# Performance work log

Hardware: AMD Instinct MI355X
Metric: run time of the kernel (lower is better)

The kernel has to match this reference:

```python
import jax, jax.numpy as jnp
import numpy as np

D = 2048      # d_model
H = 16        # n_heads
DH = 128      # head dim
ROPE = 64     # qk_rope_dim = dh//2
NOPE = 64     # qk_nope_dim = dh//2
QP = 1024     # q_proj_dim = int(D*0.5)
KVP = 1365    # kv_proj_dim = int(D*2/3)
THETA = 10000.0
B, S = 2, 2048


def _ln(x, w, b):
    m = x.mean(-1, keepdims=True)
    v = ((x - m) ** 2).mean(-1, keepdims=True)
    return (x - m) / jnp.sqrt(v + 1e-5) * w + b


def _rot_half(x):
    x1, x2 = jnp.split(x, 2, axis=-1)
    return jnp.concatenate([-x2, x1], axis=-1)


def _rope_tables(seq_len):
    # freqs over full dh (as in torch buffer), then slice first ROPE//2 and repeat(...,2)
    freqs = 1.0 / (THETA ** (jnp.arange(0, DH, 2, dtype=jnp.float32) / DH))  # (DH//2,)
    emb = jnp.arange(seq_len, dtype=jnp.float32)[:, None] * freqs[None, :]   # (S, DH//2)
    c = jnp.cos(emb)[:, : ROPE // 2]
    s = jnp.sin(emb)[:, : ROPE // 2]
    cos = jnp.concatenate([c, c], axis=-1)  # (S, ROPE)  matches .repeat(1,1,1,2)
    sin = jnp.concatenate([s, s], axis=-1)
    return cos, sin


def setup_inputs() -> dict:
    ks = jax.random.split(jax.random.key(0), 8)
    p = lambda i, shape: 0.01 * jax.random.normal(ks[i], shape, dtype=jnp.float32)
    return {
        "query": jax.random.normal(ks[0], (B, S, D), dtype=jnp.float32),
        "W_dq": p(1, (D, QP)),
        "W_uq": p(2, (QP, D)),
        "q_ln_w": jnp.ones((QP,), jnp.float32),
        "q_ln_b": jnp.zeros((QP,), jnp.float32),
        "W_dkv": p(3, (D, KVP + ROPE)),
        "W_ukv": p(4, (KVP, D + H * NOPE)),
        "kv_ln_w": jnp.ones((KVP,), jnp.float32),
        "kv_ln_b": jnp.zeros((KVP,), jnp.float32),
        "W_o": p(5, (D, D)),
    }


def reference(query, W_dq, W_uq, q_ln_w, q_ln_b, W_dkv, W_ukv, kv_ln_w, kv_ln_b, W_o):
    b, sq, _ = query.shape
    # Q low-rank path
    cq = _ln(query @ W_dq, q_ln_w, q_ln_b)                       # (B,S,QP)
    Q = (cq @ W_uq).reshape(b, sq, H, DH).transpose(0, 2, 1, 3)  # (B,H,S,DH)
    Qn, Qr = Q[..., :NOPE], Q[..., NOPE:]
    cos, sin = _rope_tables(sq)                                  # (S,ROPE)
    Qr = Qr * cos + _rot_half(Qr) * sin
    # KV low-rank path
    compressed_kv = query @ W_dkv                                # (B,S,KVP+ROPE)
    kv_lat, Kr = compressed_kv[..., :KVP], compressed_kv[..., KVP:]
    kv_lat = _ln(kv_lat, kv_ln_w, kv_ln_b)
    KV = (kv_lat @ W_ukv).reshape(b, sq, H, DH + NOPE).transpose(0, 2, 1, 3)
    Kn, V = KV[..., :NOPE], KV[..., NOPE:]                       # (B,H,S,NOPE),(B,H,S,DH)
    Kr = Kr * cos + _rot_half(Kr) * sin                          # (B,S,ROPE) shared head
    qh = jnp.concatenate([Qn, Qr], axis=-1)                      # (B,H,S,DH)
    kh = jnp.concatenate([Kn, jnp.broadcast_to(Kr[:, None], (b, H, sq, ROPE))], axis=-1)
    # causal attention, scale 1/sqrt(dh) as in SDPA
    scores = jnp.einsum('bhqd,bhkd->bhqk', qh, kh) / jnp.sqrt(jnp.float32(DH))
    mask = jnp.tril(jnp.ones((sq, sq), dtype=bool))
    scores = jnp.where(mask, scores, -jnp.inf)
    attn = jax.nn.softmax(scores, axis=-1)
    out = jnp.einsum('bhqk,bhkd->bhqd', attn, V).transpose(0, 2, 1, 3).reshape(b, sq, D)
    output = out @ W_o.T                                          # nn.Linear, no bias
    return output, compressed_kv
```

## Files before the change

### kernel.cpp

```cpp
#include <hip/hip_runtime.h>

#define BB_   2
#define S_    2048
#define D_    2048
#define H_    16
#define DH_   128
#define ROPE_ 64
#define QP_   1024
#define KVP_  1365
#define KVPR_ 1429
#define KVP_PAD_ 1408
#define NKV_PAD_ 1536
#define NCOMB_ 2560
#define MT_   4096
#define UKV_N_ 3072

typedef unsigned short u16;
typedef unsigned int   u32;
typedef __attribute__((ext_vector_type(8))) u16    u16x8;
typedef __attribute__((ext_vector_type(8))) __bf16 bf16x8;
typedef __attribute__((ext_vector_type(4))) float  f32x4;

#define NEG_BIG (-1.0e30f)
#define F32_FLAG_BITS 0x49742400u

__device__ __forceinline__ float bf2f(u16 u) {
    u32 x = ((u32)u) << 16;
    return __builtin_bit_cast(float, x);
}
__device__ __forceinline__ u16 f2bf(float f) {
    u32 u = __builtin_bit_cast(u32, f);
    u32 r = u + 0x7fffu + ((u >> 16) & 1u);
    return (u16)(r >> 16);
}
__device__ __forceinline__ bf16x8 ld_bf8(const u16* p) {
    u16x8 v = *(const u16x8*)p;
    return __builtin_bit_cast(bf16x8, v);
}
__device__ __forceinline__ bool flag_f32(const u32* flag) { return flag[0] > F32_FLAG_BITS; }

__device__ __forceinline__ void async16(const void* g, void* l) {
    __builtin_amdgcn_global_load_lds(
        (const __attribute__((address_space(1))) void*)g,
        (__attribute__((address_space(3))) void*)l, 16, 0, 0);
}

__global__ __launch_bounds__(256) void detect_kernel(const u16* __restrict__ q, u32* __restrict__ flag)
{
    u32 m = 0;
    for (int i = blockIdx.x * 256 + threadIdx.x; i < (1 << 20); i += 64 * 256) {
        float v = fabsf(bf2f(q[i]));
        u32 b = __builtin_bit_cast(u32, v);
        m = m > b ? m : b;
    }
    #pragma unroll
    for (int off = 32; off; off >>= 1) {
        u32 o = (u32)__shfl_xor((int)m, off, 64);
        m = m > o ? m : o;
    }
    if ((threadIdx.x & 63) == 0) atomicMax(flag, m);
}

__global__ __launch_bounds__(256) void cast_bf16_kernel(
    const void* __restrict__ in, u16* __restrict__ out, long n, const u32* __restrict__ flag)
{
    bool f32 = flag_f32(flag);
    long i0 = ((long)blockIdx.x * 256 + threadIdx.x) * 8;
    if (i0 >= n) return;
    u16x8 o;
    if (f32) {
        const float* p = (const float*)in + i0;
        #pragma unroll
        for (int j = 0; j < 8; j++) o[j] = f2bf(p[j]);
    } else {
        o = *(const u16x8*)((const u16*)in + i0);
    }
    *(u16x8*)(out + i0) = o;
}

template <int MODE>
__global__ __launch_bounds__(256) void gemm_bt(
    const u16* __restrict__ A, const u16* __restrict__ Bt,
    void* __restrict__ Cout, int M, int N, int K, const u32* __restrict__ flag)
{
    __shared__ u16 As[2][128 * 32];
    __shared__ u16 Bs[2][128 * 32];
    const int tid  = threadIdx.x;
    const int lane = tid & 63;
    const int wave = tid >> 6;
    const int m0 = blockIdx.x * 128;
    const int n0 = blockIdx.y * 128;
    const int wr = (wave >> 1) * 64;
    const int wc = (wave & 1) * 64;
    const bool f32o = (MODE == 2) ? flag_f32(flag) : false;

    const int srow = lane >> 2;
    const int scol = (lane & 3) * 8;
    const u16* aptr0 = A  + (long)(m0 + wave * 32 + srow) * K + scol;
    const u16* bptr0 = Bt + (long)(n0 + wave * 32 + srow) * K + scol;
    const int woff = (wave * 32) * 32;

    f32x4 acc[4][4] = {};

    const int row16 = lane & 15;
    const int kq = (lane >> 4) * 8;

    auto stage = [&](int buf, int kt) {
        u16* asl = &As[buf][woff];
        u16* bsl = &Bs[buf][woff];
        async16(aptr0 + kt,          asl);
        async16(aptr0 + 16 * K + kt, asl + 16 * 32);
        async16(bptr0 + kt,          bsl);
        async16(bptr0 + 16 * K + kt, bsl + 16 * 32);
    };
    auto compute = [&](int buf) {
        bf16x8 a[4], b[4];
        #pragma unroll
        for (int i = 0; i < 4; i++)
            a[i] = ld_bf8(&As[buf][(wr + i * 16 + row16) * 32 + kq]);
        #pragma unroll
        for (int j = 0; j < 4; j++)
            b[j] = ld_bf8(&Bs[buf][(wc + j * 16 + row16) * 32 + kq]);
        #pragma unroll
        for (int i = 0; i < 4; i++)
            #pragma unroll
            for (int j = 0; j < 4; j++)
                acc[i][j] = __builtin_amdgcn_mfma_f32_16x16x32_bf16(a[i], b[j], acc[i][j], 0, 0, 0);
    };

    stage(0, 0);
    __syncthreads();
    const int nk = K >> 5;
    for (int t = 0; t < nk; t += 2) {
        stage(1, (t + 1) * 32);
        compute(0);
        __syncthreads();
        if (t + 2 < nk) stage(0, (t + 2) * 32);
        compute(1);
        __syncthreads();
    }

    const int crow = wr + (lane >> 4) * 4;
    const int ccol = wc + row16;
    #pragma unroll
    for (int i = 0; i < 4; i++) {
        #pragma unroll
        for (int r = 0; r < 4; r++) {
            long row = m0 + crow + i * 16 + r;
            #pragma unroll
            for (int j = 0; j < 4; j++) {
                float v = acc[i][j][r];
                long col = n0 + ccol + j * 16;
                if (MODE == 2 && f32o) ((float*)Cout)[row * N + col] = v;
                else                   ((u16*)Cout)[row * N + col] = f2bf(v);
            }
        }
    }
}

__global__ __launch_bounds__(256) void transpose_pad_kernel(
    const void* __restrict__ in, u16* __restrict__ out,
    int Rin, int Cin, int Nout, int Kpad, const u32* __restrict__ flag)
{
    __shared__ u16 t[32][33];
    bool f32 = flag_f32(flag);
    int k0 = blockIdx.x * 32, n0 = blockIdx.y * 32;
    int tx = threadIdx.x & 31, ty = threadIdx.x >> 5;
    #pragma unroll
    for (int rr = 0; rr < 4; ++rr) {
        int k = k0 + ty + rr * 8, n = n0 + tx;
        u16 v = 0;
        if (k < Rin && n < Cin)
            v = f32 ? f2bf(((const float*)in)[(long)k * Cin + n])
                    : ((const u16*)in)[(long)k * Cin + n];
        t[ty + rr * 8][tx] = v;
    }
    __syncthreads();
    #pragma unroll
    for (int rr = 0; rr < 4; ++rr) {
        int n = n0 + ty + rr * 8, k = k0 + tx;
        if (n < Nout && k < Kpad) out[(long)n * Kpad + k] = t[tx][ty + rr * 8];
    }
}

__device__ __forceinline__ float block_sum(float v, float* red) {
    #pragma unroll
    for (int off = 32; off; off >>= 1) v += __shfl_xor(v, off, 64);
    int wv = threadIdx.x >> 6;
    __syncthreads();
    if ((threadIdx.x & 63) == 0) red[wv] = v;
    __syncthreads();
    return red[0] + red[1] + red[2] + red[3];
}

__global__ __launch_bounds__(256) void ln_q_kernel(
    const u16* __restrict__ x, const void* __restrict__ w, const void* __restrict__ bb,
    u16* __restrict__ y, const u32* __restrict__ flag, int stride)
{
    __shared__ float red[4];
    bool f32 = flag_f32(flag);
    long row = blockIdx.x;
    const u16* xr = x + row * stride;
    float v[4]; float s = 0.f;
    #pragma unroll
    for (int i = 0; i < 4; i++) { v[i] = bf2f(xr[threadIdx.x + i * 256]); s += v[i]; }
    float mean = block_sum(s, red) * (1.0f / QP_);
    float var = 0.f;
    #pragma unroll
    for (int i = 0; i < 4; i++) { float d = v[i] - mean; var += d * d; }
    var = block_sum(var, red) * (1.0f / QP_);
    float rstd = rsqrtf(var + 1e-5f);
    #pragma unroll
    for (int i = 0; i < 4; i++) {
        int idx = threadIdx.x + i * 256;
        float wv = f32 ? ((const float*)w)[idx] : bf2f(((const u16*)w)[idx]);
        float bv = f32 ? ((const float*)bb)[idx] : bf2f(((const u16*)bb)[idx]);
        y[row * QP_ + idx] = f2bf((v[i] - mean) * rstd * wv + bv);
    }
}

__global__ __launch_bounds__(256) void ln_kv_kernel(
    const u16* __restrict__ x, const void* __restrict__ w, const void* __restrict__ bb,
    u16* __restrict__ kv_lat, void* __restrict__ d_out, const u32* __restrict__ flag, int stride)
{
    __shared__ float red[4];
    bool f32 = flag_f32(flag);
    long row = blockIdx.x;
    const u16* xr = x + row * stride;
    u16 u[6]; float v[6]; float s = 0.f;
    #pragma unroll
    for (int i = 0; i < 6; i++) {
        int idx = threadIdx.x + i * 256;
        u[i] = xr[idx];
        v[i] = bf2f(u[i]);
        if (idx < KVP_) s += v[i];
    }
    float mean = block_sum(s, red) * (1.0f / KVP_);
    float var = 0.f;
    #pragma unroll
    for (int i = 0; i < 6; i++) {
        int idx = threadIdx.x + i * 256;
        if (idx < KVP_) { float d = v[i] - mean; var += d * d; }
    }
    var = block_sum(var, red) * (1.0f / KVP_);
    float rstd = rsqrtf(var + 1e-5f);

    float* out1f = (float*)d_out + (size_t)MT_ * D_;
    u16*   out1h = (u16*)d_out   + (size_t)MT_ * D_;
    #pragma unroll
    for (int i = 0; i < 6; i++) {
        int idx = threadIdx.x + i * 256;
        if (idx < KVPR_) {
            if (f32) out1f[row * KVPR_ + idx] = v[i];
            else     out1h[row * KVPR_ + idx] = u[i];
        }
        if (idx < KVP_PAD_) {
            float wv = 0.f, bv = 0.f;
            if (idx < KVP_) {
                wv = f32 ? ((const float*)w)[idx] : bf2f(((const u16*)w)[idx]);
                bv = f32 ? ((const float*)bb)[idx] : bf2f(((const u16*)bb)[idx]);
            }
            u16 o = 0;
            if (idx < KVP_) o = f2bf((v[i] - mean) * rstd * wv + bv);
            kv_lat[row * KVP_PAD_ + idx] = o;
        }
    }
}

__global__ void rope_tab_kernel(float* __restrict__ cosT, float* __restrict__ sinT, u32* __restrict__ flag) {
    int idx = blockIdx.x * 256 + threadIdx.x;
    if (idx == 0) flag[0] = 0u;
    if (idx >= S_ * 32) return;
    int pos = idx >> 5, i = idx & 31;
    float freq = (float)exp(-((double)i / 64.0) * log(10000.0));
    float ang = (float)pos * freq;
    cosT[idx] = (float)cos((double)ang);
    sinT[idx] = (float)sin((double)ang);
}

__global__ __launch_bounds__(256) void pack_q_kernel(
    const u16* __restrict__ Qm, const float* __restrict__ cosT, const float* __restrict__ sinT,
    u16* __restrict__ qh)
{
    int bs = blockIdx.x; int b = bs >> 11; int s = bs & 2047;
    int h = threadIdx.x >> 4; int d0 = (threadIdx.x & 15) * 8;
    const u16* src = Qm + (long)bs * 2048 + h * 128 + d0;
    u16x8 val = *(const u16x8*)src;
    if (d0 >= 64) {
        int r0 = d0 - 64;
        const u16* rb = Qm + (long)bs * 2048 + h * 128 + 64;
        u16x8 out;
        #pragma unroll
        for (int j = 0; j < 8; j++) {
            int r = r0 + j; int m = r & 31;
            float c = cosT[s * 32 + m], sn = sinT[s * 32 + m];
            float x = bf2f(val[j]);
            float o = (r < 32) ? -bf2f(rb[r + 32]) : bf2f(rb[r - 32]);
            out[j] = f2bf(x * c + o * sn);
        }
        val = out;
    }
    *(u16x8*)&qh[(((long)(b * H_ + h)) * S_ + s) * 128 + d0] = val;
}

__global__ __launch_bounds__(256) void pack_kh_kernel(
    const u16* __restrict__ KV, const void* __restrict__ d_out,
    const float* __restrict__ cosT, const float* __restrict__ sinT,
    u16* __restrict__ kh, const u32* __restrict__ flag)
{
    bool f32 = flag_f32(flag);
    int bs = blockIdx.x; int b = bs >> 11; int s = bs & 2047;
    int h = threadIdx.x >> 4; int d0 = (threadIdx.x & 15) * 8;
    u16x8 val;
    if (d0 < 64) {
        val = *(const u16x8*)&KV[(long)bs * 3072 + h * 192 + d0];
    } else {
        int r0 = d0 - 64;
        const float* rf = (const float*)d_out + (size_t)MT_ * D_ + (long)bs * KVPR_ + KVP_;
        const u16*   rh = (const u16*)d_out   + (size_t)MT_ * D_ + (long)bs * KVPR_ + KVP_;
        #pragma unroll
        for (int j = 0; j < 8; j++) {
            int r = r0 + j; int m = r & 31;
            float xr = f32 ? rf[r] : bf2f(rh[r]);
            float xo = f32 ? ((r < 32) ? -rf[r + 32] : rf[r - 32])
                           : ((r < 32) ? -bf2f(rh[r + 32]) : bf2f(rh[r - 32]));
            val[j] = f2bf(xr * cosT[s * 32 + m] + xo * sinT[s * 32 + m]);
        }
    }
    *(u16x8*)&kh[(((long)(b * H_ + h)) * S_ + s) * 128 + d0] = val;
}

__global__ __launch_bounds__(256) void pack_vt_kernel(const u16* __restrict__ KV, u16* __restrict__ Vt)
{
    int bh = blockIdx.x; int b = bh >> 4, h = bh & 15;
    int s0 = blockIdx.y * 64;
    __shared__ u16 t[64][136];
    #pragma unroll
    for (int it = 0; it < 4; ++it) {
        int ch = threadIdx.x + it * 256;
        int sr = ch >> 4, c8 = (ch & 15) * 8;
        *(u16x8*)&t[sr][c8] = *(const u16x8*)&KV[((long)(b * S_ + s0 + sr)) * 3072 + h * 192 + 64 + c8];
    }
    __syncthreads();
    #pragma unroll
    for (int it = 0; it < 4; ++it) {
        int ch = threadIdx.x + it * 256;
        int d = ch >> 3, s8 = (ch & 7) * 8;
        u16x8 v;
        #pragma unroll
        for (int j = 0; j < 8; j++) v[j] = t[s8 + j][d];
        *(u16x8*)&Vt[((long)bh * 128 + d) * S_ + s0 + s8] = v;
    }
}

#define ATT_SCALE 0.08838834764831845f
#define K_LOG2E (ATT_SCALE * 1.4426950408889634f)
#define DEFER_THR 62.0f

__global__ __launch_bounds__(512, 4) void attn_kernel(
    const u16* __restrict__ qh, const u16* __restrict__ kh,
    const u16* __restrict__ Vt, u16* __restrict__ attn_out)
{
    __shared__ u16 Ks[64 * 128];
    __shared__ u16 Vs[144 * 64];
    __shared__ u16 Ps[8][16 * 72];

    const int bh = (int)blockIdx.x + ((int)blockIdx.z << 3);
    const int b = bh >> 4, h = bh & 15;
    const int jq = 15 - (int)blockIdx.y;
    const int qbase = jq * 128;
    const int tid = threadIdx.x;
    const int lane = tid & 63;
    const int w = tid >> 6;
    const int row16 = lane & 15;
    const int quad = lane >> 4;
    const int kq = quad * 8;
    u16* Psw = Ps[w];

    for (int i = tid; i < 16 * 64; i += 512)
        Vs[128 * 64 + i] = (i < 64) ? (u16)0x3F80 : (u16)0;

    bf16x8 aq[4];
    const long qrow = (long)bh * S_ + qbase + w * 16 + row16;
    #pragma unroll
    for (int kc = 0; kc < 4; kc++)
        aq[kc] = ld_bf8(&qh[qrow * 128 + kc * 32 + kq]);

    f32x4 o[9] = {};
    float m_run[4];
    #pragma unroll
    for (int r = 0; r < 4; r++) m_run[r] = NEG_BIG;

    const long khb = (long)bh * S_;
    const int kend = qbase + 128;

    u16x8 kst[2], vst[2];
    auto load_kv = [&](int k0) {
        #pragma unroll
        for (int it = 0; it < 2; ++it) {
            int r = w * 8 + it * 4 + (lane >> 4);
            kst[it] = *(const u16x8*)&kh[(khb + k0 + r) * 128 + (((lane & 15) ^ (r & 7)) << 3)];
        }
        #pragma unroll
        for (int it = 0; it < 2; ++it) {
            int d = w * 16 + it * 8 + (lane >> 3);
            vst[it] = *(const u16x8*)&Vt[((long)bh * 128 + d) * S_ + k0 + (((lane & 7) ^ (d & 7)) << 3)];
        }
    };

    load_kv(0);

    for (int k0 = 0; k0 < kend; k0 += 64) {
        __syncthreads();
        #pragma unroll
        for (int it = 0; it < 2; ++it)
            *(u16x8*)&Ks[(w * 8 + it * 4) * 128 + lane * 8] = kst[it];
        #pragma unroll
        for (int it = 0; it < 2; ++it)
            *(u16x8*)&Vs[(w * 16 + it * 8) * 64 + lane * 8] = vst[it];
        __syncthreads();
        if (k0 + 64 < kend) load_kv(k0 + 64);

        f32x4 sc[4] = {};
        #pragma unroll
        for (int kc = 0; kc < 4; kc++) {
            #pragma unroll
            for (int ct = 0; ct < 4; ct++) {
                bf16x8 kf = ld_bf8(&Ks[(ct * 16 + row16) * 128 +
                                       (((kc * 4 + quad) ^ (row16 & 7)) << 3)]);
                sc[ct] = __builtin_amdgcn_mfma_f32_16x16x32_bf16(aq[kc], kf, sc[ct], 0, 0, 0);
            }
        }

        const bool need_mask = (k0 >= qbase);
        float mrow[4];
        bool ok = true;
        #pragma unroll
        for (int r = 0; r < 4; r++) {
            if (need_mask) {
                int row = qbase + w * 16 + quad * 4 + r;
                sc[0][r] = (k0 + row16      <= row) ? sc[0][r] : NEG_BIG;
                sc[1][r] = (k0 + 16 + row16 <= row) ? sc[1][r] : NEG_BIG;
                sc[2][r] = (k0 + 32 + row16 <= row) ? sc[2][r] : NEG_BIG;
                sc[3][r] = (k0 + 48 + row16 <= row) ? sc[3][r] : NEG_BIG;
            }
            float m = fmaxf(fmaxf(sc[0][r], sc[1][r]), fmaxf(sc[2][r], sc[3][r]));
            #pragma unroll
            for (int off = 8; off; off >>= 1) m = fmaxf(m, __shfl_xor(m, off, 64));
            mrow[r] = m;
            ok = ok && (m <= m_run[r] + DEFER_THR);
        }
        if (!__all((int)ok)) {
            #pragma unroll
            for (int r = 0; r < 4; r++) {
                float mn = fmaxf(m_run[r], mrow[r]);
                float alpha = exp2f((m_run[r] - mn) * K_LOG2E);
                m_run[r] = mn;
                #pragma unroll
                for (int nt = 0; nt < 9; nt++) o[nt][r] *= alpha;
            }
        }
        #pragma unroll
        for (int r = 0; r < 4; r++) {
            float mk = m_run[r] * K_LOG2E;
            int prow = (quad * 4 + r) * 72;
            Psw[prow + row16]      = f2bf(exp2f(fmaf(sc[0][r], K_LOG2E, -mk)));
            Psw[prow + 16 + row16] = f2bf(exp2f(fmaf(sc[1][r], K_LOG2E, -mk)));
            Psw[prow + 32 + row16] = f2bf(exp2f(fmaf(sc[2][r], K_LOG2E, -mk)));
            Psw[prow + 48 + row16] = f2bf(exp2f(fmaf(sc[3][r], K_LOG2E, -mk)));
        }

        asm volatile("s_waitcnt lgkmcnt(0)" ::: "memory");

        #pragma unroll
        for (int kc2 = 0; kc2 < 2; kc2++) {
            bf16x8 pf = ld_bf8(&Psw[row16 * 72 + kc2 * 32 + kq]);
            #pragma unroll
            for (int nt = 0; nt < 9; nt++) {
                bf16x8 vf = ld_bf8(&Vs[(nt * 16 + row16) * 64 +
                                       (((kc2 * 4 + quad) ^ (row16 & 7)) << 3)]);
                o[nt] = __builtin_amdgcn_mfma_f32_16x16x32_bf16(pf, vf, o[nt], 0, 0, 0);
            }
        }
    }

    #pragma unroll
    for (int r = 0; r < 4; r++) {
        float l = __shfl(o[8][r], quad << 4, 64);
        float inv = 1.0f / l;
        long row = (long)b * S_ + qbase + w * 16 + quad * 4 + r;
        #pragma unroll
        for (int nt = 0; nt < 8; nt++)
            attn_out[row * 2048 + h * 128 + nt * 16 + row16] = f2bf(o[nt][r] * inv);
    }
}

#define MIB(x) ((size_t)(x) << 20)
extern "C" void kernel_launch(void* const* d_in, const int* in_sizes, int n_in,
                              void* d_out, int out_size, void* d_ws, size_t ws_size,
                              hipStream_t stream)
{
    const void* query  = d_in[0];
    const void* W_dq   = d_in[1];
    const void* W_uq   = d_in[2];
    const void* q_ln_w = d_in[3];
    const void* q_ln_b = d_in[4];
    const void* W_dkv  = d_in[5];
    const void* W_ukv  = d_in[6];
    const void* kv_ln_w = d_in[7];
    const void* kv_ln_b = d_in[8];
    const void* W_o    = d_in[9];
    (void)ws_size; (void)in_sizes; (void)n_in; (void)out_size;

    char* base = (char*)d_ws;
    u32*   flag     = (u32*)base;
    float* rope_cos = (float*)(base + 4096);
    float* rope_sin = (float*)(base + 266240);
    u16* qh     = (u16*)(base + MIB(1));
    u16* kh     = (u16*)(base + MIB(17));
    u16* Vt     = (u16*)(base + MIB(33));
    u16* q_bf   = (u16*)(base + MIB(49));
    u16* Wo_bf  = (u16*)(base + MIB(65));
    u16* Wcomb  = (u16*)(base + MIB(73));
    u16* cqkv   = (u16*)(base + MIB(83));
    u16* cq     = (u16*)(base + MIB(103));
    u16* kv_lat = (u16*)(base + MIB(111));
    u16* WuqT   = (u16*)(base + MIB(73));
    u16* Qmat   = (u16*)(base + MIB(77));
    u16* WukvT  = (u16*)(base + MIB(73));
    u16* KV     = (u16*)(base + MIB(82));
    u16* attn_o = (u16*)(base + MIB(106));

    rope_tab_kernel<<<(S_ * 32 + 255) / 256, 256, 0, stream>>>(rope_cos, rope_sin, flag);
    detect_kernel<<<64, 256, 0, stream>>>((const u16*)query, flag);

    cast_bf16_kernel<<<4096, 256, 0, stream>>>(query, q_bf, (long)MT_ * D_, flag);
    cast_bf16_kernel<<<2048, 256, 0, stream>>>(W_o, Wo_bf, (long)D_ * D_, flag);

    transpose_pad_kernel<<<dim3(64, 32), 256, 0, stream>>>(W_dq, Wcomb, 2048, 1024, 1024, 2048, flag);
    transpose_pad_kernel<<<dim3(64, 48), 256, 0, stream>>>(W_dkv, Wcomb + (size_t)1024 * 2048, 2048, KVPR_, NKV_PAD_, 2048, flag);
    gemm_bt<0><<<dim3(32, 20), 256, 0, stream>>>(q_bf, Wcomb, cqkv, MT_, NCOMB_, D_, flag);
    ln_q_kernel<<<MT_, 256, 0, stream>>>(cqkv, q_ln_w, q_ln_b, cq, flag, NCOMB_);
    ln_kv_kernel<<<MT_, 256, 0, stream>>>(cqkv + 1024, kv_ln_w, kv_ln_b, kv_lat, d_out, flag, NCOMB_);

    transpose_pad_kernel<<<dim3(32, 64), 256, 0, stream>>>(W_uq, WuqT, 1024, 2048, 2048, 1024, flag);
    gemm_bt<0><<<dim3(32, 16), 256, 0, stream>>>(cq, WuqT, Qmat, MT_, D_, QP_, flag);
    pack_q_kernel<<<MT_, 256, 0, stream>>>(Qmat, rope_cos, rope_sin, qh);

    transpose_pad_kernel<<<dim3(44, 96), 256, 0, stream>>>(W_ukv, WukvT, KVP_, UKV_N_, UKV_N_, KVP_PAD_, flag);
    gemm_bt<0><<<dim3(32, 24), 256, 0, stream>>>(kv_lat, WukvT, KV, MT_, UKV_N_, KVP_PAD_, flag);
    pack_kh_kernel<<<MT_, 256, 0, stream>>>(KV, d_out, rope_cos, rope_sin, kh, flag);
    pack_vt_kernel<<<dim3(32, 32), 256, 0, stream>>>(KV, Vt);

    attn_kernel<<<dim3(8, 16, 4), 512, 0, stream>>>(qh, kh, Vt, attn_o);
    gemm_bt<2><<<dim3(32, 16), 256, 0, stream>>>(attn_o, Wo_bf, d_out, MT_, D_, D_, flag);
}
```

Baseline: 556.6 us.

## Rewrite attention with 32x32 MFMA, transposed scores, and register-resident P

The attention kernel now uses 4 waves of 32 query rows each and 32x32x16 bf16 MFMA tiles. It computes S^T = K·Q^T so the probabilities stay in registers and are repacked via lane shuffles into the PV operand, removing the LDS P buffer. The ones-column trick for the row sum is replaced by an explicit l_run accumulation, and waves skip fully masked KV tiles. This cuts LDS traffic and MFMA instruction count, but halves threads per block and raises register pressure.

```diff
diff --git a/kernel.cpp b/kernel.cpp
--- a/kernel.cpp
+++ b/kernel.cpp
@@ -17,9 +17,12 @@
 
 typedef unsigned short u16;
 typedef unsigned int   u32;
+typedef __attribute__((ext_vector_type(4))) u16    u16x4;
 typedef __attribute__((ext_vector_type(8))) u16    u16x8;
+typedef __attribute__((ext_vector_type(4))) u32    u32x4;
 typedef __attribute__((ext_vector_type(8))) __bf16 bf16x8;
 typedef __attribute__((ext_vector_type(4))) float  f32x4;
+typedef __attribute__((ext_vector_type(16))) float f32x16;
 
 #define NEG_BIG (-1.0e30f)
 #define F32_FLAG_BITS 0x49742400u
@@ -32,6 +35,10 @@
     u32 u = __builtin_bit_cast(u32, f);
     u32 r = u + 0x7fffu + ((u >> 16) & 1u);
     return (u16)(r >> 16);
+}
+__device__ __forceinline__ u32 pk2(float a, float b) {
+    __bf16 x = (__bf16)a, y = (__bf16)b;
+    return (u32)__builtin_bit_cast(u16, x) | ((u32)__builtin_bit_cast(u16, y) << 16);
 }
 __device__ __forceinline__ bf16x8 ld_bf8(const u16* p) {
     u16x8 v = *(const u16x8*)p;
@@ -357,13 +364,12 @@
 #define K_LOG2E (ATT_SCALE * 1.4426950408889634f)
 #define DEFER_THR 62.0f
 
-__global__ __launch_bounds__(512, 4) void attn_kernel(
+__global__ __launch_bounds__(256, 2) void attn_kernel(
     const u16* __restrict__ qh, const u16* __restrict__ kh,
     const u16* __restrict__ Vt, u16* __restrict__ attn_out)
 {
     __shared__ u16 Ks[64 * 128];
-    __shared__ u16 Vs[144 * 64];
-    __shared__ u16 Ps[8][16 * 72];
+    __shared__ u16 Vs[128 * 64];
 
     const int bh = (int)blockIdx.x + ((int)blockIdx.z << 3);
     const int b = bh >> 4, h = bh & 15;
@@ -372,38 +378,37 @@
     const int tid = threadIdx.x;
     const int lane = tid & 63;
     const int w = tid >> 6;
-    const int row16 = lane & 15;
-    const int quad = lane >> 4;
-    const int kq = quad * 8;
-    u16* Psw = Ps[w];
-
-    for (int i = tid; i < 16 * 64; i += 512)
-        Vs[128 * 64 + i] = (i < 64) ? (u16)0x3F80 : (u16)0;
-
-    bf16x8 aq[4];
-    const long qrow = (long)bh * S_ + qbase + w * 16 + row16;
-    #pragma unroll
-    for (int kc = 0; kc < 4; kc++)
-        aq[kc] = ld_bf8(&qh[qrow * 128 + kc * 32 + kq]);
-
-    f32x4 o[9] = {};
-    float m_run[4];
-    #pragma unroll
-    for (int r = 0; r < 4; r++) m_run[r] = NEG_BIG;
+    const int l5 = lane & 31;
+    const int hi = lane >> 5;
+    const int wq0 = qbase + w * 32;
+    const int qg = wq0 + l5;
+    const int kend = qbase + 128;
+    const int kend_w = wq0 + 32;
+
+    bf16x8 qb[8];
+    {
+        const u16* qp = &qh[((long)bh * S_ + qg) * 128 + 8 * hi];
+        #pragma unroll
+        for (int kc = 0; kc < 8; kc++)
+            qb[kc] = ld_bf8(qp + kc * 16);
+    }
+
+    f32x16 o[4] = {};
+    float m_run = NEG_BIG;
+    float l_run = 0.f;
 
     const long khb = (long)bh * S_;
-    const int kend = qbase + 128;
-
-    u16x8 kst[2], vst[2];
+
+    u16x8 kst[4], vst[4];
     auto load_kv = [&](int k0) {
         #pragma unroll
-        for (int it = 0; it < 2; ++it) {
-            int r = w * 8 + it * 4 + (lane >> 4);
+        for (int it = 0; it < 4; ++it) {
+            int r = w * 16 + it * 4 + (lane >> 4);
             kst[it] = *(const u16x8*)&kh[(khb + k0 + r) * 128 + (((lane & 15) ^ (r & 7)) << 3)];
         }
         #pragma unroll
-        for (int it = 0; it < 2; ++it) {
-            int d = w * 16 + it * 8 + (lane >> 3);
+        for (int it = 0; it < 4; ++it) {
+            int d = w * 32 + it * 8 + (lane >> 3);
             vst[it] = *(const u16x8*)&Vt[((long)bh * 128 + d) * S_ + k0 + (((lane & 7) ^ (d & 7)) << 3)];
         }
     };
@@ -413,86 +418,106 @@
     for (int k0 = 0; k0 < kend; k0 += 64) {
         __syncthreads();
         #pragma unroll
-        for (int it = 0; it < 2; ++it)
-            *(u16x8*)&Ks[(w * 8 + it * 4) * 128 + lane * 8] = kst[it];
-        #pragma unroll
-        for (int it = 0; it < 2; ++it)
-            *(u16x8*)&Vs[(w * 16 + it * 8) * 64 + lane * 8] = vst[it];
+        for (int it = 0; it < 4; ++it)
+            *(u16x8*)&Ks[(w * 16 + it * 4) * 128 + lane * 8] = kst[it];
+        #pragma unroll
+        for (int it = 0; it < 4; ++it)
+            *(u16x8*)&Vs[(w * 32 + it * 8) * 64 + lane * 8] = vst[it];
         __syncthreads();
         if (k0 + 64 < kend) load_kv(k0 + 64);
 
-        f32x4 sc[4] = {};
-        #pragma unroll
-        for (int kc = 0; kc < 4; kc++) {
-            #pragma unroll
-            for (int ct = 0; ct < 4; ct++) {
-                bf16x8 kf = ld_bf8(&Ks[(ct * 16 + row16) * 128 +
-                                       (((kc * 4 + quad) ^ (row16 & 7)) << 3)]);
-                sc[ct] = __builtin_amdgcn_mfma_f32_16x16x32_bf16(aq[kc], kf, sc[ct], 0, 0, 0);
+        if (k0 < kend_w) {
+            f32x16 sc[2] = {};
+            #pragma unroll
+            for (int kc = 0; kc < 8; kc++) {
+                #pragma unroll
+                for (int ct = 0; ct < 2; ct++) {
+                    int krow = ct * 32 + l5;
+                    bf16x8 kf = ld_bf8(&Ks[krow * 128 + (((2 * kc + hi) ^ (krow & 7)) << 3)]);
+                    sc[ct] = __builtin_amdgcn_mfma_f32_32x32x16_bf16(kf, qb[kc], sc[ct], 0, 0, 0);
+                }
             }
-        }
-
-        const bool need_mask = (k0 >= qbase);
-        float mrow[4];
-        bool ok = true;
-        #pragma unroll
-        for (int r = 0; r < 4; r++) {
-            if (need_mask) {
-                int row = qbase + w * 16 + quad * 4 + r;
-                sc[0][r] = (k0 + row16      <= row) ? sc[0][r] : NEG_BIG;
-                sc[1][r] = (k0 + 16 + row16 <= row) ? sc[1][r] : NEG_BIG;
-                sc[2][r] = (k0 + 32 + row16 <= row) ? sc[2][r] : NEG_BIG;
-                sc[3][r] = (k0 + 48 + row16 <= row) ? sc[3][r] : NEG_BIG;
+            if (k0 + 64 > wq0) {
+                #pragma unroll
+                for (int ct = 0; ct < 2; ct++)
+                    #pragma unroll
+                    for (int g = 0; g < 4; g++)
+                        #pragma unroll
+                        for (int t = 0; t < 4; t++)
+                            sc[ct][g * 4 + t] =
+                                (k0 + ct * 32 + g * 8 + t + 4 * hi <= qg) ? sc[ct][g * 4 + t] : NEG_BIG;
             }
-            float m = fmaxf(fmaxf(sc[0][r], sc[1][r]), fmaxf(sc[2][r], sc[3][r]));
-            #pragma unroll
-            for (int off = 8; off; off >>= 1) m = fmaxf(m, __shfl_xor(m, off, 64));
-            mrow[r] = m;
-            ok = ok && (m <= m_run[r] + DEFER_THR);
-        }
-        if (!__all((int)ok)) {
-            #pragma unroll
-            for (int r = 0; r < 4; r++) {
-                float mn = fmaxf(m_run[r], mrow[r]);
-                float alpha = exp2f((m_run[r] - mn) * K_LOG2E);
-                m_run[r] = mn;
+            float m = sc[0][0];
+            #pragma unroll
+            for (int i = 1; i < 16; i++) m = fmaxf(m, sc[0][i]);
+            #pragma unroll
+            for (int i = 0; i < 16; i++) m = fmaxf(m, sc[1][i]);
+            m = fmaxf(m, __shfl_xor(m, 32, 64));
+            bool ok = (m <= m_run + DEFER_THR);
+            if (!__all((int)ok)) {
+                float mn = fmaxf(m_run, m);
+                float alpha = exp2f((m_run - mn) * K_LOG2E);
+                m_run = mn;
+                l_run *= alpha;
                 #pragma unroll
-                for (int nt = 0; nt < 9; nt++) o[nt][r] *= alpha;
+                for (int dt = 0; dt < 4; dt++)
+                    #pragma unroll
+                    for (int i = 0; i < 16; i++) o[dt][i] *= alpha;
             }
-        }
-        #pragma unroll
-        for (int r = 0; r < 4; r++) {
-            float mk = m_run[r] * K_LOG2E;
-            int prow = (quad * 4 + r) * 72;
-            Psw[prow + row16]      = f2bf(exp2f(fmaf(sc[0][r], K_LOG2E, -mk)));
-            Psw[prow + 16 + row16] = f2bf(exp2f(fmaf(sc[1][r], K_LOG2E, -mk)));
-            Psw[prow + 32 + row16] = f2bf(exp2f(fmaf(sc[2][r], K_LOG2E, -mk)));
-            Psw[prow + 48 + row16] = f2bf(exp2f(fmaf(sc[3][r], K_LOG2E, -mk)));
-        }
-
-        asm volatile("s_waitcnt lgkmcnt(0)" ::: "memory");
-
-        #pragma unroll
-        for (int kc2 = 0; kc2 < 2; kc2++) {
-            bf16x8 pf = ld_bf8(&Psw[row16 * 72 + kc2 * 32 + kq]);
-            #pragma unroll
-            for (int nt = 0; nt < 9; nt++) {
-                bf16x8 vf = ld_bf8(&Vs[(nt * 16 + row16) * 64 +
-                                       (((kc2 * 4 + quad) ^ (row16 & 7)) << 3)]);
-                o[nt] = __builtin_amdgcn_mfma_f32_16x16x32_bf16(pf, vf, o[nt], 0, 0, 0);
+            float mk = m_run * K_LOG2E;
+            float s = 0.f;
+            #pragma unroll
+            for (int ct = 0; ct < 2; ct++)
+                #pragma unroll
+                for (int i = 0; i < 16; i++) {
+                    float p = exp2f(fmaf(sc[ct][i], K_LOG2E, -mk));
+                    sc[ct][i] = p;
+                    s += p;
+                }
+            l_run += s + __shfl_xor(s, 32, 64);
+            bf16x8 pb[4];
+            #pragma unroll
+            for (int ct = 0; ct < 2; ct++)
+                #pragma unroll
+                for (int c2 = 0; c2 < 2; c2++) {
+                    u32 lo0 = pk2(sc[ct][8 * c2 + 0], sc[ct][8 * c2 + 1]);
+                    u32 lo1 = pk2(sc[ct][8 * c2 + 2], sc[ct][8 * c2 + 3]);
+                    u32 h0  = pk2(sc[ct][8 * c2 + 4], sc[ct][8 * c2 + 5]);
+                    u32 h1  = pk2(sc[ct][8 * c2 + 6], sc[ct][8 * c2 + 7]);
+                    u32 s0 = hi ? lo0 : h0;
+                    u32 s1 = hi ? lo1 : h1;
+                    u32 r0 = (u32)__shfl_xor((int)s0, 32, 64);
+                    u32 r1 = (u32)__shfl_xor((int)s1, 32, 64);
+                    u32x4 f;
+                    f[0] = hi ? r0 : lo0;
+                    f[1] = hi ? r1 : lo1;
+                    f[2] = hi ? h0 : r0;
+                    f[3] = hi ? h1 : r1;
+                    pb[ct * 2 + c2] = __builtin_bit_cast(bf16x8, f);
+                }
+            #pragma unroll
+            for (int kk = 0; kk < 4; kk++) {
+                #pragma unroll
+                for (int dt = 0; dt < 4; dt++) {
+                    int drow = dt * 32 + l5;
+                    bf16x8 vf = ld_bf8(&Vs[drow * 64 + (((2 * kk + hi) ^ (drow & 7)) << 3)]);
+                    o[dt] = __builtin_amdgcn_mfma_f32_32x32x16_bf16(vf, pb[kk], o[dt], 0, 0, 0);
+                }
             }
         }
     }
 
-    #pragma unroll
-    for (int r = 0; r < 4; r++) {
-        float l = __shfl(o[8][r], quad << 4, 64);
-        float inv = 1.0f / l;
-        long row = (long)b * S_ + qbase + w * 16 + quad * 4 + r;
-        #pragma unroll
-        for (int nt = 0; nt < 8; nt++)
-            attn_out[row * 2048 + h * 128 + nt * 16 + row16] = f2bf(o[nt][r] * inv);
-    }
+    float inv = 1.0f / l_run;
+    const long orow = ((long)b * S_ + qg) * 2048 + h * 128;
+    #pragma unroll
+    for (int dt = 0; dt < 4; dt++)
+        #pragma unroll
+        for (int g = 0; g < 4; g++) {
+            u16x4 v;
+            #pragma unroll
+            for (int t = 0; t < 4; t++) v[t] = f2bf(o[dt][g * 4 + t] * inv);
+            *(u16x4*)&attn_out[orow + dt * 32 + g * 8 + 4 * hi] = v;
+        }
 }
 
 #define MIB(x) ((size_t)(x) << 20)
@@ -552,6 +577,6 @@
     pack_kh_kernel<<<MT_, 256, 0, stream>>>(KV, d_out, rope_cos, rope_sin, kh, flag);
     pack_vt_kernel<<<dim3(32, 32), 256, 0, stream>>>(KV, Vt);
 
-    attn_kernel<<<dim3(8, 16, 4), 512, 0, stream>>>(qh, kh, Vt, attn_o);
+    attn_kernel<<<dim3(8, 16, 4), 256, 0, stream>>>(qh, kh, Vt, attn_o);
     gemm_bt<2><<<dim3(32, 16), 256, 0, stream>>>(attn_o, Wo_bf, d_out, MT_, D_, D_, flag);
 }
```

After: 524.4 us. 1.06x faster.
